# Performance work log

Measured on AMD Instinct MI355X. Metric: run time of the kernel, lower is better.

## Reference

```python
import jax, jax.numpy as jnp
import numpy as np

N, E, D, H, FE = 50000, 800000, 256, 8, 64
HD = D // H  # head_dim = 32


def setup_inputs() -> dict:
    key = jax.random.key(0)
    ks = jax.random.split(key, 14)
    sD = 1.0 / np.sqrt(D)
    sF = 1.0 / np.sqrt(FE)
    return {
        "h": jax.random.normal(ks[0], (N, D), jnp.float32),
        "efeat": jax.random.normal(ks[1], (E, FE), jnp.float32),
        "src": jax.random.randint(ks[2], (E,), 0, N),
        "dst": jax.random.randint(ks[3], (E,), 0, N),
        "Wq": jax.random.normal(ks[4], (D, D), jnp.float32) * sD,
        "Wk": jax.random.normal(ks[5], (D, D), jnp.float32) * sD,
        "Wv": jax.random.normal(ks[6], (D, D), jnp.float32) * sD,
        "W1": jax.random.normal(ks[7], (FE, D), jnp.float32) * sF,
        "b1": jnp.zeros((D,), jnp.float32),
        "W2": jax.random.normal(ks[8], (D, H), jnp.float32) * sD,
        "b2": jnp.zeros((H,), jnp.float32),
        "Wo": jax.random.normal(ks[9], (D, D), jnp.float32) * sD,
        "bo": jnp.zeros((D,), jnp.float32),
    }


def reference(h, efeat, src, dst, Wq, Wk, Wv, W1, b1, W2, b2, Wo, bo):
    n = h.shape[0]
    # node projections, split into heads: (N, H, HD)
    Q = (h @ Wq).reshape(n, H, HD)
    K = (h @ Wk).reshape(n, H, HD)
    V = (h @ Wv).reshape(n, H, HD)
    # per-edge scaled dot-product score (E, H)
    score = jnp.einsum("ehd,ehd->eh", Q[dst], K[src]) / np.sqrt(HD)
    # edge MLP bias: Linear -> ReLU -> Linear, (E, H)
    score = score + jax.nn.relu(efeat @ W1 + b1) @ W2 + b2
    # segment softmax over incoming edges of each dst node
    m = jax.ops.segment_max(score, dst, num_segments=n)        # (N, H)
    ex = jnp.exp(score - m[dst])                               # (E, H)
    denom = jax.ops.segment_sum(ex, dst, num_segments=n)      # (N, H)
    alpha = ex / denom[dst]                                    # (E, H)
    # scatter weighted sum of source V into dst nodes
    out = jax.ops.segment_sum(alpha[:, :, None] * V[src], dst, num_segments=n)
    out = out.reshape(n, D)  # nodes with no in-edges stay zero (matches DGL)
    return out @ Wo + bo
```

## Files before the change

kernel.cpp:

```cpp
#include <hip/hip_runtime.h>
#include <math.h>


typedef short s8v __attribute__((ext_vector_type(8)));
typedef float f32x4 __attribute__((ext_vector_type(4)));

__device__ inline unsigned short f2bf(float x) {
    unsigned int u = __float_as_uint(x);
    unsigned int r = u + 0x7FFFu + ((u >> 16) & 1u);
    return (unsigned short)(r >> 16);
}
__device__ inline float bf2f(unsigned short b) {
    return __uint_as_float(((unsigned int)b) << 16);
}

__global__ __launch_bounds__(256) void gemm256(const float* __restrict__ A,
                                               const float* __restrict__ W,
                                               const float* __restrict__ bias,
                                               float* __restrict__ C, int M) {
    const int K = 256;
    __shared__ float As[16][68];
    __shared__ float Ws[16][68];
    int t  = threadIdx.x;
    int bm = blockIdx.x * 64;
    int bn = blockIdx.y * 64;
    int tx = t & 15, ty = t >> 4;
    float acc[4][4] = {};

    int la_m = t >> 2;
    int la_k = (t & 3) * 4;
    int lw_k = t >> 4;
    int lw_n = (t & 15) * 4;

    for (int k0 = 0; k0 < K; k0 += 16) {
        float4 av;
        int gm = bm + la_m;
        if (gm < M) av = *(const float4*)&A[(size_t)gm * K + k0 + la_k];
        else        av = make_float4(0.f, 0.f, 0.f, 0.f);
        As[la_k + 0][la_m] = av.x;
        As[la_k + 1][la_m] = av.y;
        As[la_k + 2][la_m] = av.z;
        As[la_k + 3][la_m] = av.w;
        float4 wv = *(const float4*)&W[(size_t)(k0 + lw_k) * K + bn + lw_n];
        *(float4*)&Ws[lw_k][lw_n] = wv;
        __syncthreads();
#pragma unroll
        for (int kk = 0; kk < 16; ++kk) {
            float4 a4 = *(const float4*)&As[kk][ty * 4];
            float4 w4 = *(const float4*)&Ws[kk][tx * 4];
            float am[4] = {a4.x, a4.y, a4.z, a4.w};
            float wn[4] = {w4.x, w4.y, w4.z, w4.w};
#pragma unroll
            for (int i = 0; i < 4; ++i)
#pragma unroll
                for (int j = 0; j < 4; ++j)
                    acc[i][j] += am[i] * wn[j];
        }
        __syncthreads();
    }
#pragma unroll
    for (int i = 0; i < 4; ++i) {
        int gm = bm + ty * 4 + i;
        if (gm >= M) continue;
#pragma unroll
        for (int j = 0; j < 4; ++j) {
            int gn = bn + tx * 4 + j;
            float v = acc[i][j];
            if (bias) v += bias[gn];
            C[(size_t)gm * 256 + gn] = v;
        }
    }
}

__global__ void prep_w1(const float* __restrict__ W1,
                        unsigned short* __restrict__ W1h,
                        unsigned short* __restrict__ W1l) {
    int f = blockIdx.x * 256 + threadIdx.x;
    if (f >= 16384) return;
    int i    = f & 7;
    int lane = (f >> 3) & 63;
    int nc   = (f >> 9) & 15;
    int kc   = (f >> 13) & 1;
    int k    = kc * 32 + (lane >> 4) * 8 + i;
    int col  = nc * 16 + (lane & 15);
    float v = W1[k * 256 + col];
    unsigned short hb = f2bf(v);
    W1h[f] = hb;
    W1l[f] = f2bf(v - bf2f(hb));
}

__global__ void prep_w2(const float* __restrict__ W2,
                        unsigned short* __restrict__ W2f) {
    int f = blockIdx.x * 256 + threadIdx.x;
    if (f >= 4096) return;
    int i    = f & 7;
    int lane = (f >> 3) & 63;
    int kc   = (f >> 9) & 7;
    int k    = kc * 32 + (lane >> 4) * 8 + i;
    int col  = lane & 15;
    float v = (col < 8) ? W2[k * 8 + col] : 0.f;
    W2f[f] = f2bf(v);
}

__global__ __launch_bounds__(256) void edge_mlp_mfma(
        const float* __restrict__ efeat,
        const unsigned short* __restrict__ W1h,
        const unsigned short* __restrict__ W1l,
        const unsigned short* __restrict__ W2f,
        const float* __restrict__ b1, const float* __restrict__ b2,
        float* __restrict__ mlp, int E) {
    __shared__ float efs[64][68];
    __shared__ unsigned short hid[64][264];
    __shared__ float b1s[256];
    int t  = threadIdx.x;
    int e0 = blockIdx.x * 64;

    {
        int row = t >> 2, cq = (t & 3) * 16;
        int ge = e0 + row;
#pragma unroll
        for (int u = 0; u < 4; ++u) {
            float4 v;
            if (ge < E) v = *(const float4*)&efeat[(size_t)ge * 64 + cq + u * 4];
            else        v = make_float4(0.f, 0.f, 0.f, 0.f);
            *(float4*)&efs[row][cq + u * 4] = v;
        }
        b1s[t] = b1[t];
    }
    __syncthreads();

    int w = t >> 6;
    int l = t & 63;
    int c = l & 15, g = l >> 4;

    s8v Ah[4][2], Al[4][2];
#pragma unroll
    for (int m = 0; m < 4; ++m) {
        int row = m * 16 + c;
#pragma unroll
        for (int kc = 0; kc < 2; ++kc) {
            const float* p = &efs[row][kc * 32 + g * 8];
            float x[8];
            *(float4*)&x[0] = *(const float4*)&p[0];
            *(float4*)&x[4] = *(const float4*)&p[4];
            s8v hi, lo;
#pragma unroll
            for (int i = 0; i < 8; ++i) {
                unsigned short hb = f2bf(x[i]);
                hi[i] = (short)hb;
                lo[i] = (short)f2bf(x[i] - bf2f(hb));
            }
            Ah[m][kc] = hi;
            Al[m][kc] = lo;
        }
    }

    f32x4 acc[4][4];
#pragma unroll
    for (int m = 0; m < 4; ++m)
#pragma unroll
        for (int n = 0; n < 4; ++n)
            acc[m][n] = f32x4{0.f, 0.f, 0.f, 0.f};

#pragma unroll
    for (int ncl = 0; ncl < 4; ++ncl) {
        int nc = w * 4 + ncl;
        s8v Bh[2], Bl[2];
#pragma unroll
        for (int kc = 0; kc < 2; ++kc) {
            size_t base = ((size_t)((kc * 16 + nc) * 64 + l)) * 8;
            Bh[kc] = *(const s8v*)&W1h[base];
            Bl[kc] = *(const s8v*)&W1l[base];
        }
#pragma unroll
        for (int m = 0; m < 4; ++m) {
#pragma unroll
            for (int kc = 0; kc < 2; ++kc) {
                acc[m][ncl] = __builtin_amdgcn_mfma_f32_16x16x32_bf16(Ah[m][kc], Bh[kc], acc[m][ncl], 0, 0, 0);
                acc[m][ncl] = __builtin_amdgcn_mfma_f32_16x16x32_bf16(Ah[m][kc], Bl[kc], acc[m][ncl], 0, 0, 0);
                acc[m][ncl] = __builtin_amdgcn_mfma_f32_16x16x32_bf16(Al[m][kc], Bh[kc], acc[m][ncl], 0, 0, 0);
            }
        }
    }

#pragma unroll
    for (int m = 0; m < 4; ++m) {
#pragma unroll
        for (int ncl = 0; ncl < 4; ++ncl) {
            int j = w * 64 + ncl * 16 + c;
            float bj = b1s[j];
#pragma unroll
            for (int r = 0; r < 4; ++r) {
                int e = m * 16 + g * 4 + r;
                float v = fmaxf(acc[m][ncl][r] + bj, 0.f);
                hid[e][j] = f2bf(v);
            }
        }
    }
    __syncthreads();

    f32x4 acc2 = f32x4{0.f, 0.f, 0.f, 0.f};
#pragma unroll
    for (int kc = 0; kc < 8; ++kc) {
        s8v a = *(const s8v*)&hid[w * 16 + c][kc * 32 + g * 8];
        s8v b = *(const s8v*)&W2f[(size_t)(kc * 64 + l) * 8];
        acc2 = __builtin_amdgcn_mfma_f32_16x16x32_bf16(a, b, acc2, 0, 0, 0);
    }
    if (c < 8) {
        float bb = b2[c];
#pragma unroll
        for (int r = 0; r < 4; ++r) {
            int ge = e0 + w * 16 + g * 4 + r;
            if (ge < E) mlp[(size_t)ge * 8 + c] = acc2[r] + bb;
        }
    }
}

__global__ void count_edges(const int* __restrict__ dst, int* counts, int E) {
    int e = blockIdx.x * 256 + threadIdx.x;
    if (e < E) atomicAdd(&counts[dst[e]], 1);
}

__global__ __launch_bounds__(1024) void scan_counts(const int* __restrict__ counts,
                                                    int* indptr, int* fill, int n) {
    __shared__ int sm[1024];
    __shared__ int carry_s;
    int t = threadIdx.x;
    if (t == 0) carry_s = 0;
    __syncthreads();
    for (int base = 0; base < n; base += 1024) {
        int i = base + t;
        int v = (i < n) ? counts[i] : 0;
        sm[t] = v;
        __syncthreads();
        for (int off = 1; off < 1024; off <<= 1) {
            int u = (t >= off) ? sm[t - off] : 0;
            __syncthreads();
            sm[t] += u;
            __syncthreads();
        }
        int carry = carry_s;
        int excl  = carry + sm[t] - v;
        if (i < n) { indptr[i] = excl; fill[i] = excl; }
        __syncthreads();
        if (t == 1023) carry_s = carry + sm[1023];
        __syncthreads();
    }
    if (t == 0) indptr[n] = carry_s;
}

__global__ void scatter_edges(const int* __restrict__ dst, int* fill,
                              int* edge_ids, int E) {
    int e = blockIdx.x * 256 + threadIdx.x;
    if (e < E) {
        int pos = atomicAdd(&fill[dst[e]], 1);
        edge_ids[pos] = e;
    }
}

__global__ __launch_bounds__(64) void node_aggregate(
        const float* __restrict__ Q, const float* __restrict__ K,
        const float* __restrict__ V, const float* __restrict__ mlp,
        const float* __restrict__ b2, const int* __restrict__ src,
        const int* __restrict__ indptr, const int* __restrict__ edge_ids,
        float* __restrict__ outp, int Nn) {
    int b = blockIdx.x;
    if (b >= Nn) return;
    int lane = threadIdx.x;
    int g = lane >> 3;
    float4 q4 = *(const float4*)&Q[(size_t)b * 256 + lane * 4];
    int beg = indptr[b], end = indptr[b + 1];
    float o0 = 0.f, o1 = 0.f, o2 = 0.f, o3 = 0.f;
    float den = 0.f;
    const float inv_sqrt = 0.17677669529663687f;
    for (int idx = beg; idx < end; ++idx) {
        int e = edge_ids[idx];
        int s = src[e];
        float4 k4 = *(const float4*)&K[(size_t)s * 256 + lane * 4];
        float4 v4 = *(const float4*)&V[(size_t)s * 256 + lane * 4];
        float part = q4.x * k4.x + q4.y * k4.y + q4.z * k4.z + q4.w * k4.w;
        part += __shfl_xor(part, 1, 64);
        part += __shfl_xor(part, 2, 64);
        part += __shfl_xor(part, 4, 64);
        float scv = part * inv_sqrt + mlp[(size_t)e * 8 + g];
        float p = __expf(scv);
        den += p;
        o0 += p * v4.x; o1 += p * v4.y; o2 += p * v4.z; o3 += p * v4.w;
    }
    float invd = (end > beg) ? 1.f / den : 0.f;
    float4 ov = make_float4(o0 * invd, o1 * invd, o2 * invd, o3 * invd);
    *(float4*)&outp[(size_t)b * 256 + lane * 4] = ov;
}

extern "C" void kernel_launch(void* const* d_in, const int* in_sizes, int n_in,
                              void* d_out, int out_size, void* d_ws, size_t ws_size,
                              hipStream_t stream) {
    const float* h     = (const float*)d_in[0];
    const float* efeat = (const float*)d_in[1];
    const int*   src   = (const int*)d_in[2];
    const int*   dst   = (const int*)d_in[3];
    const float* Wq    = (const float*)d_in[4];
    const float* Wk    = (const float*)d_in[5];
    const float* Wv    = (const float*)d_in[6];
    const float* W1    = (const float*)d_in[7];
    const float* b1    = (const float*)d_in[8];
    const float* W2    = (const float*)d_in[9];
    const float* b2    = (const float*)d_in[10];
    const float* Wo    = (const float*)d_in[11];
    const float* bo    = (const float*)d_in[12];
    float* out = (float*)d_out;

    const int N = in_sizes[0] / 256;
    const int E = in_sizes[2];

    char* p = (char*)d_ws;
    auto carve = [&](size_t bytes) {
        char* r = p;
        p += (bytes + 255) & ~(size_t)255;
        return (void*)r;
    };
    float* Q      = (float*)carve((size_t)N * 256 * 4);
    float* Kp     = (float*)carve((size_t)N * 256 * 4);
    float* Vp     = (float*)carve((size_t)N * 256 * 4);
    float* mlp    = (float*)carve((size_t)E * 8 * 4);
    float* outp   = (float*)carve((size_t)N * 256 * 4);
    int* counts   = (int*)carve((size_t)N * 4);
    int* indptr   = (int*)carve((size_t)(N + 1) * 4);
    int* fill     = (int*)carve((size_t)N * 4);
    int* edge_ids = (int*)carve((size_t)E * 4);
    unsigned short* W1h = (unsigned short*)carve(16384 * 2);
    unsigned short* W1l = (unsigned short*)carve(16384 * 2);
    unsigned short* W2f = (unsigned short*)carve(4096 * 2);

    hipMemsetAsync(counts, 0, (size_t)N * 4, stream);

    prep_w1<<<64, 256, 0, stream>>>(W1, W1h, W1l);
    prep_w2<<<16, 256, 0, stream>>>(W2, W2f);

    dim3 gg((N + 63) / 64, 4);
    gemm256<<<gg, 256, 0, stream>>>(h, Wq, nullptr, Q, N);
    gemm256<<<gg, 256, 0, stream>>>(h, Wk, nullptr, Kp, N);
    gemm256<<<gg, 256, 0, stream>>>(h, Wv, nullptr, Vp, N);
    edge_mlp_mfma<<<(E + 63) / 64, 256, 0, stream>>>(efeat, W1h, W1l, W2f, b1, b2, mlp, E);
    count_edges<<<(E + 255) / 256, 256, 0, stream>>>(dst, counts, E);
    scan_counts<<<1, 1024, 0, stream>>>(counts, indptr, fill, N);
    scatter_edges<<<(E + 255) / 256, 256, 0, stream>>>(dst, fill, edge_ids, E);
    node_aggregate<<<N, 64, 0, stream>>>(Q, Kp, Vp, mlp, b2, src, indptr, edge_ids, outp, N);
    gemm256<<<gg, 256, 0, stream>>>(outp, Wo, bo, out, N);
}
```

Measured before the change: 1.248 ms.

## Move node GEMMs to split-bf16 MFMA, store K/V as bf16, CSR-ordered edge data

```diff
diff --git a/kernel.cpp b/kernel.cpp
--- a/kernel.cpp
+++ b/kernel.cpp
@@ -14,60 +14,106 @@
     return __uint_as_float(((unsigned int)b) << 16);
 }
 
-__global__ __launch_bounds__(256) void gemm256(const float* __restrict__ A,
-                                               const float* __restrict__ W,
-                                               const float* __restrict__ bias,
-                                               float* __restrict__ C, int M) {
-    const int K = 256;
-    __shared__ float As[16][68];
-    __shared__ float Ws[16][68];
-    int t  = threadIdx.x;
-    int bm = blockIdx.x * 64;
-    int bn = blockIdx.y * 64;
-    int tx = t & 15, ty = t >> 4;
-    float acc[4][4] = {};
-
-    int la_m = t >> 2;
-    int la_k = (t & 3) * 4;
-    int lw_k = t >> 4;
-    int lw_n = (t & 15) * 4;
-
-    for (int k0 = 0; k0 < K; k0 += 16) {
-        float4 av;
-        int gm = bm + la_m;
-        if (gm < M) av = *(const float4*)&A[(size_t)gm * K + k0 + la_k];
-        else        av = make_float4(0.f, 0.f, 0.f, 0.f);
-        As[la_k + 0][la_m] = av.x;
-        As[la_k + 1][la_m] = av.y;
-        As[la_k + 2][la_m] = av.z;
-        As[la_k + 3][la_m] = av.w;
-        float4 wv = *(const float4*)&W[(size_t)(k0 + lw_k) * K + bn + lw_n];
-        *(float4*)&Ws[lw_k][lw_n] = wv;
-        __syncthreads();
-#pragma unroll
-        for (int kk = 0; kk < 16; ++kk) {
-            float4 a4 = *(const float4*)&As[kk][ty * 4];
-            float4 w4 = *(const float4*)&Ws[kk][tx * 4];
-            float am[4] = {a4.x, a4.y, a4.z, a4.w};
-            float wn[4] = {w4.x, w4.y, w4.z, w4.w};
-#pragma unroll
-            for (int i = 0; i < 4; ++i)
-#pragma unroll
-                for (int j = 0; j < 4; ++j)
-                    acc[i][j] += am[i] * wn[j];
-        }
-        __syncthreads();
-    }
-#pragma unroll
-    for (int i = 0; i < 4; ++i) {
-        int gm = bm + ty * 4 + i;
-        if (gm >= M) continue;
+__global__ __launch_bounds__(256) void prep_split(const float* __restrict__ X,
+                                                  unsigned short* __restrict__ Xh,
+                                                  unsigned short* __restrict__ Xl,
+                                                  int n4) {
+    for (int i = blockIdx.x * 256 + threadIdx.x; i < n4; i += gridDim.x * 256) {
+        float4 v = ((const float4*)X)[i];
+        ushort4 hv, lv;
+        float x[4] = {v.x, v.y, v.z, v.w};
+        unsigned short hh[4], ll[4];
 #pragma unroll
         for (int j = 0; j < 4; ++j) {
-            int gn = bn + tx * 4 + j;
-            float v = acc[i][j];
-            if (bias) v += bias[gn];
-            C[(size_t)gm * 256 + gn] = v;
+            hh[j] = f2bf(x[j]);
+            ll[j] = f2bf(x[j] - bf2f(hh[j]));
+        }
+        hv.x = hh[0]; hv.y = hh[1]; hv.z = hh[2]; hv.w = hh[3];
+        lv.x = ll[0]; lv.y = ll[1]; lv.z = ll[2]; lv.w = ll[3];
+        ((ushort4*)Xh)[i] = hv;
+        ((ushort4*)Xl)[i] = lv;
+    }
+}
+
+__global__ void prep_w256(const float* __restrict__ W,
+                          unsigned short* __restrict__ Wh,
+                          unsigned short* __restrict__ Wl) {
+    int f = blockIdx.x * 256 + threadIdx.x;
+    if (f >= 65536) return;
+    int i    = f & 7;
+    int lane = (f >> 3) & 63;
+    int nc   = (f >> 9) & 15;
+    int kc   = f >> 13;
+    int k    = kc * 32 + (lane >> 4) * 8 + i;
+    int col  = nc * 16 + (lane & 15);
+    float v = W[k * 256 + col];
+    unsigned short hb = f2bf(v);
+    Wh[f] = hb;
+    Wl[f] = f2bf(v - bf2f(hb));
+}
+
+__global__ __launch_bounds__(256) void gemm_mfma(
+        const unsigned short* __restrict__ Ah, const unsigned short* __restrict__ Al,
+        const unsigned short* __restrict__ Wh, const unsigned short* __restrict__ Wl,
+        const float* __restrict__ bias,
+        float* __restrict__ outF,
+        unsigned short* __restrict__ outB, int ob_stride, int ob_off,
+        int M) {
+    int t = threadIdx.x;
+    int w = t >> 6, l = t & 63;
+    int c = l & 15, g = l >> 4;
+    int row0 = blockIdx.x * 64;
+
+    f32x4 acc[4][4];
+#pragma unroll
+    for (int m = 0; m < 4; ++m)
+#pragma unroll
+        for (int n = 0; n < 4; ++n) acc[m][n] = f32x4{0.f, 0.f, 0.f, 0.f};
+
+#pragma unroll
+    for (int kc = 0; kc < 8; ++kc) {
+        s8v ah[4], al[4];
+#pragma unroll
+        for (int m = 0; m < 4; ++m) {
+            int row = row0 + m * 16 + c;
+            if (row < M) {
+                size_t off = (size_t)row * 256 + kc * 32 + g * 8;
+                ah[m] = *(const s8v*)&Ah[off];
+                al[m] = *(const s8v*)&Al[off];
+            } else {
+                ah[m] = s8v{0, 0, 0, 0, 0, 0, 0, 0};
+                al[m] = s8v{0, 0, 0, 0, 0, 0, 0, 0};
+            }
+        }
+#pragma unroll
+        for (int n = 0; n < 4; ++n) {
+            int nc = w * 4 + n;
+            size_t bo = ((size_t)(kc * 16 + nc) * 64 + l) * 8;
+            s8v bh = *(const s8v*)&Wh[bo];
+            s8v bl = *(const s8v*)&Wl[bo];
+#pragma unroll
+            for (int m = 0; m < 4; ++m) {
+                acc[m][n] = __builtin_amdgcn_mfma_f32_16x16x32_bf16(ah[m], bh, acc[m][n], 0, 0, 0);
+                acc[m][n] = __builtin_amdgcn_mfma_f32_16x16x32_bf16(ah[m], bl, acc[m][n], 0, 0, 0);
+                acc[m][n] = __builtin_amdgcn_mfma_f32_16x16x32_bf16(al[m], bh, acc[m][n], 0, 0, 0);
+            }
+        }
+    }
+
+#pragma unroll
+    for (int m = 0; m < 4; ++m) {
+#pragma unroll
+        for (int n = 0; n < 4; ++n) {
+            int col = w * 64 + n * 16 + c;
+            float bb = bias ? bias[col] : 0.f;
+#pragma unroll
+            for (int r = 0; r < 4; ++r) {
+                int row = row0 + m * 16 + g * 4 + r;
+                if (row >= M) continue;
+                float v = acc[m][n][r] + bb;
+                if (outF) outF[(size_t)row * 256 + col] = v;
+                if (outB) outB[(size_t)row * ob_stride + ob_off + col] = f2bf(v);
+            }
         }
     }
 }
@@ -108,7 +154,8 @@
         const unsigned short* __restrict__ W1l,
         const unsigned short* __restrict__ W2f,
         const float* __restrict__ b1, const float* __restrict__ b2,
-        float* __restrict__ mlp, int E) {
+        const int* __restrict__ pos_of_edge,
+        float* __restrict__ mlp_csr, int E) {
     __shared__ float efs[64][68];
     __shared__ unsigned short hid[64][264];
     __shared__ float b1s[256];
@@ -159,8 +206,7 @@
 #pragma unroll
     for (int m = 0; m < 4; ++m)
 #pragma unroll
-        for (int n = 0; n < 4; ++n)
-            acc[m][n] = f32x4{0.f, 0.f, 0.f, 0.f};
+        for (int n = 0; n < 4; ++n) acc[m][n] = f32x4{0.f, 0.f, 0.f, 0.f};
 
 #pragma unroll
     for (int ncl = 0; ncl < 4; ++ncl) {
@@ -211,7 +257,10 @@
 #pragma unroll
         for (int r = 0; r < 4; ++r) {
             int ge = e0 + w * 16 + g * 4 + r;
-            if (ge < E) mlp[(size_t)ge * 8 + c] = acc2[r] + bb;
+            if (ge < E) {
+                int p = pos_of_edge[ge];
+                mlp_csr[(size_t)p * 8 + c] = acc2[r] + bb;
+            }
         }
     }
 }
@@ -224,72 +273,78 @@
 __global__ __launch_bounds__(1024) void scan_counts(const int* __restrict__ counts,
                                                     int* indptr, int* fill, int n) {
     __shared__ int sm[1024];
-    __shared__ int carry_s;
     int t = threadIdx.x;
-    if (t == 0) carry_s = 0;
+    int per = (n + 1023) / 1024;
+    int b = t * per, e = min(b + per, n);
+    int s = 0;
+    for (int i = b; i < e; ++i) s += counts[i];
+    sm[t] = s;
     __syncthreads();
-    for (int base = 0; base < n; base += 1024) {
-        int i = base + t;
-        int v = (i < n) ? counts[i] : 0;
-        sm[t] = v;
+    for (int off = 1; off < 1024; off <<= 1) {
+        int u = (t >= off) ? sm[t - off] : 0;
         __syncthreads();
-        for (int off = 1; off < 1024; off <<= 1) {
-            int u = (t >= off) ? sm[t - off] : 0;
-            __syncthreads();
-            sm[t] += u;
-            __syncthreads();
-        }
-        int carry = carry_s;
-        int excl  = carry + sm[t] - v;
-        if (i < n) { indptr[i] = excl; fill[i] = excl; }
+        sm[t] += u;
         __syncthreads();
-        if (t == 1023) carry_s = carry + sm[1023];
-        __syncthreads();
-    }
-    if (t == 0) indptr[n] = carry_s;
-}
-
-__global__ void scatter_edges(const int* __restrict__ dst, int* fill,
-                              int* edge_ids, int E) {
+    }
+    int excl = t ? sm[t - 1] : 0;
+    for (int i = b; i < e; ++i) {
+        indptr[i] = excl;
+        fill[i]   = excl;
+        excl += counts[i];
+    }
+    if (t == 1023) indptr[n] = sm[1023];
+}
+
+__global__ void scatter_edges(const int* __restrict__ dst, const int* __restrict__ src,
+                              int* fill, int* pos_of_edge, int* src_s, int E) {
     int e = blockIdx.x * 256 + threadIdx.x;
     if (e < E) {
         int pos = atomicAdd(&fill[dst[e]], 1);
-        edge_ids[pos] = e;
-    }
-}
-
-__global__ __launch_bounds__(64) void node_aggregate(
-        const float* __restrict__ Q, const float* __restrict__ K,
-        const float* __restrict__ V, const float* __restrict__ mlp,
-        const float* __restrict__ b2, const int* __restrict__ src,
-        const int* __restrict__ indptr, const int* __restrict__ edge_ids,
-        float* __restrict__ outp, int Nn) {
-    int b = blockIdx.x;
-    if (b >= Nn) return;
-    int lane = threadIdx.x;
-    int g = lane >> 3;
-    float4 q4 = *(const float4*)&Q[(size_t)b * 256 + lane * 4];
-    int beg = indptr[b], end = indptr[b + 1];
-    float o0 = 0.f, o1 = 0.f, o2 = 0.f, o3 = 0.f;
-    float den = 0.f;
+        pos_of_edge[e] = pos;
+        src_s[pos] = src[e];
+    }
+}
+
+__global__ __launch_bounds__(256) void node_aggregate2(
+        const float* __restrict__ Q, const unsigned short* __restrict__ KVb,
+        const float* __restrict__ mlp_csr, const int* __restrict__ src_s,
+        const int* __restrict__ indptr, float* __restrict__ outp, int Nn) {
+    int node = blockIdx.x * 4 + (threadIdx.x >> 6);
+    if (node >= Nn) return;
+    int l = threadIdx.x & 63;
+    int g = l >> 3;
+    float4 q4 = *(const float4*)&Q[(size_t)node * 256 + l * 4];
+    int beg = indptr[node], end = indptr[node + 1];
+    float o0 = 0.f, o1 = 0.f, o2 = 0.f, o3 = 0.f, den = 0.f;
     const float inv_sqrt = 0.17677669529663687f;
-    for (int idx = beg; idx < end; ++idx) {
-        int e = edge_ids[idx];
-        int s = src[e];
-        float4 k4 = *(const float4*)&K[(size_t)s * 256 + lane * 4];
-        float4 v4 = *(const float4*)&V[(size_t)s * 256 + lane * 4];
-        float part = q4.x * k4.x + q4.y * k4.y + q4.z * k4.z + q4.w * k4.w;
-        part += __shfl_xor(part, 1, 64);
-        part += __shfl_xor(part, 2, 64);
-        part += __shfl_xor(part, 4, 64);
-        float scv = part * inv_sqrt + mlp[(size_t)e * 8 + g];
-        float p = __expf(scv);
-        den += p;
-        o0 += p * v4.x; o1 += p * v4.y; o2 += p * v4.z; o3 += p * v4.w;
+
+    if (beg < end) {
+        int last = end - 1;
+        int s  = src_s[beg];
+        int sn = src_s[min(beg + 1, last)];
+        ushort4 k4 = *(const ushort4*)&KVb[(size_t)s * 512 + l * 4];
+        ushort4 v4 = *(const ushort4*)&KVb[(size_t)s * 512 + 256 + l * 4];
+        for (int idx = beg; idx < end; ++idx) {
+            int scur = sn;
+            sn = src_s[min(idx + 2, last)];
+            ushort4 k4n = *(const ushort4*)&KVb[(size_t)scur * 512 + l * 4];
+            ushort4 v4n = *(const ushort4*)&KVb[(size_t)scur * 512 + 256 + l * 4];
+            float mv = mlp_csr[(size_t)idx * 8 + g];
+            float part = q4.x * bf2f(k4.x) + q4.y * bf2f(k4.y) +
+                         q4.z * bf2f(k4.z) + q4.w * bf2f(k4.w);
+            part += __shfl_xor(part, 1, 64);
+            part += __shfl_xor(part, 2, 64);
+            part += __shfl_xor(part, 4, 64);
+            float p = __expf(part * inv_sqrt + mv);
+            den += p;
+            o0 += p * bf2f(v4.x); o1 += p * bf2f(v4.y);
+            o2 += p * bf2f(v4.z); o3 += p * bf2f(v4.w);
+            k4 = k4n; v4 = v4n;
+        }
     }
     float invd = (end > beg) ? 1.f / den : 0.f;
     float4 ov = make_float4(o0 * invd, o1 * invd, o2 * invd, o3 * invd);
-    *(float4*)&outp[(size_t)b * 256 + lane * 4] = ov;
+    *(float4*)&outp[(size_t)node * 256 + l * 4] = ov;
 }
 
 extern "C" void kernel_launch(void* const* d_in, const int* in_sizes, int n_in,
@@ -319,32 +374,53 @@
         p += (bytes + 255) & ~(size_t)255;
         return (void*)r;
     };
+    unsigned short* h_hi = (unsigned short*)carve((size_t)N * 256 * 2);
+    unsigned short* h_lo = (unsigned short*)carve((size_t)N * 256 * 2);
     float* Q      = (float*)carve((size_t)N * 256 * 4);
-    float* Kp     = (float*)carve((size_t)N * 256 * 4);
-    float* Vp     = (float*)carve((size_t)N * 256 * 4);
-    float* mlp    = (float*)carve((size_t)E * 8 * 4);
+    unsigned short* KVb = (unsigned short*)carve((size_t)N * 512 * 2);
+    float* mlp_csr = (float*)carve((size_t)E * 8 * 4);
     float* outp   = (float*)carve((size_t)N * 256 * 4);
     int* counts   = (int*)carve((size_t)N * 4);
     int* indptr   = (int*)carve((size_t)(N + 1) * 4);
     int* fill     = (int*)carve((size_t)N * 4);
-    int* edge_ids = (int*)carve((size_t)E * 4);
+    int* pos_of_edge = (int*)carve((size_t)E * 4);
+    int* src_s    = (int*)carve((size_t)E * 4);
+    unsigned short* WqH = (unsigned short*)carve(65536 * 2);
+    unsigned short* WqL = (unsigned short*)carve(65536 * 2);
+    unsigned short* WkH = (unsigned short*)carve(65536 * 2);
+    unsigned short* WkL = (unsigned short*)carve(65536 * 2);
+    unsigned short* WvH = (unsigned short*)carve(65536 * 2);
+    unsigned short* WvL = (unsigned short*)carve(65536 * 2);
+    unsigned short* WoH = (unsigned short*)carve(65536 * 2);
+    unsigned short* WoL = (unsigned short*)carve(65536 * 2);
     unsigned short* W1h = (unsigned short*)carve(16384 * 2);
     unsigned short* W1l = (unsigned short*)carve(16384 * 2);
     unsigned short* W2f = (unsigned short*)carve(4096 * 2);
 
     hipMemsetAsync(counts, 0, (size_t)N * 4, stream);
 
+    prep_w256<<<256, 256, 0, stream>>>(Wq, WqH, WqL);
+    prep_w256<<<256, 256, 0, stream>>>(Wk, WkH, WkL);
+    prep_w256<<<256, 256, 0, stream>>>(Wv, WvH, WvL);
+    prep_w256<<<256, 256, 0, stream>>>(Wo, WoH, WoL);
     prep_w1<<<64, 256, 0, stream>>>(W1, W1h, W1l);
     prep_w2<<<16, 256, 0, stream>>>(W2, W2f);
 
-    dim3 gg((N + 63) / 64, 4);
-    gemm256<<<gg, 256, 0, stream>>>(h, Wq, nullptr, Q, N);
-    gemm256<<<gg, 256, 0, stream>>>(h, Wk, nullptr, Kp, N);
-    gemm256<<<gg, 256, 0, stream>>>(h, Wv, nullptr, Vp, N);
-    edge_mlp_mfma<<<(E + 63) / 64, 256, 0, stream>>>(efeat, W1h, W1l, W2f, b1, b2, mlp, E);
     count_edges<<<(E + 255) / 256, 256, 0, stream>>>(dst, counts, E);
     scan_counts<<<1, 1024, 0, stream>>>(counts, indptr, fill, N);
-    scatter_edges<<<(E + 255) / 256, 256, 0, stream>>>(dst, fill, edge_ids, E);
-    node_aggregate<<<N, 64, 0, stream>>>(Q, Kp, Vp, mlp, b2, src, indptr, edge_ids, outp, N);
-    gemm256<<<gg, 256, 0, stream>>>(outp, Wo, bo, out, N);
-}
+    scatter_edges<<<(E + 255) / 256, 256, 0, stream>>>(dst, src, fill, pos_of_edge, src_s, E);
+
+    int gx = (N + 63) / 64;
+    prep_split<<<2048, 256, 0, stream>>>(h, h_hi, h_lo, N * 64);
+    gemm_mfma<<<gx, 256, 0, stream>>>(h_hi, h_lo, WqH, WqL, nullptr, Q, nullptr, 0, 0, N);
+    gemm_mfma<<<gx, 256, 0, stream>>>(h_hi, h_lo, WkH, WkL, nullptr, nullptr, KVb, 512, 0, N);
+    gemm_mfma<<<gx, 256, 0, stream>>>(h_hi, h_lo, WvH, WvL, nullptr, nullptr, KVb, 512, 256, N);
+
+    edge_mlp_mfma<<<(E + 63) / 64, 256, 0, stream>>>(efeat, W1h, W1l, W2f, b1, b2,
+                                                     pos_of_edge, mlp_csr, E);
+
+    node_aggregate2<<<(N + 3) / 4, 256, 0, stream>>>(Q, KVb, mlp_csr, src_s, indptr, outp, N);
+
+    prep_split<<<2048, 256, 0, stream>>>(outp, h_hi, h_lo, N * 64);
+    gemm_mfma<<<gx, 256, 0, stream>>>(h_hi, h_lo, WoH, WoL, bo, out, nullptr, 0, 0, N);
+}
```

New measurement: 1.077 ms. 13.7% less time.
